# Optimization experiments

Measured on AMD Instinct MI355X. Metric: run time of the kernel, lower is better.

Reference implementation:

```python
import jax, jax.numpy as jnp
import numpy as np

B, N, L = 32, 50, 16384  # batch, n_templates, segment length
KT = 4096                # template kernel length


def conv1d(x, w, pad, groups=1):
    # x: [B, Cin, L], w: [Cout, Cin/groups, K] (torch layout)
    return jax.lax.conv_general_dilated(
        x, w, window_strides=(1,), padding=[(pad, pad)],
        dimension_numbers=('NCH', 'OIH', 'NCH'), feature_group_count=groups)


def maxpool3(x):
    # MaxPool1d(kernel=3, stride=3), floor mode (VALID)
    return jax.lax.reduce_window(x, -jnp.inf, jax.lax.max,
                                 (1, 1, 3), (1, 1, 3), 'VALID')


def pad_to(x, m):
    p = (-x.shape[-1]) % m
    pads = ((0, 0),) * (x.ndim - 1) + ((0, p),)
    return jnp.pad(x, pads)


def setup_inputs() -> dict:
    key = jax.random.key(0)
    ks = jax.random.split(key, 12)
    return dict(
        xi=jax.random.normal(ks[0], (B, 2, L), jnp.float32),
        S_t_m12=jax.random.normal(ks[1], (2, 1, L), jnp.float32) * 0.01,
        template=jax.random.normal(ks[2], (N, 2, KT), jnp.float32) * 0.01,
        hh_sqrt=jax.random.uniform(ks[3], (N, 2), jnp.float32) + 0.5,
        W1=jax.random.normal(ks[4], (16, 2, 3), jnp.float32) * 0.1,
        b1=jnp.zeros((16,), jnp.float32),
        W2=jax.random.normal(ks[5], (32, 16, 3), jnp.float32) * 0.1,
        b2=jnp.zeros((32,), jnp.float32),
        W3=jax.random.normal(ks[6], (32, 128), jnp.float32) * 0.1,
        b3=jnp.zeros((32,), jnp.float32),
        W4=jax.random.normal(ks[7], (2, 32), jnp.float32) * 0.1,
        b4=jnp.zeros((2,), jnp.float32),
    )


def reference(xi, S_t_m12, template, hh_sqrt, W1, b1, W2, b2, W3, b3, W4, b4):
    # Whitening matched filter: grouped conv with kernel length L
    y = conv1d(xi, S_t_m12, L - 1, groups=2)          # [B, 2, 2L-1]
    y = pad_to(y, L)                                   # [B, 2, 2L]
    # wrap-fold each channel: reshape(B,2,L).sum over the fold axis
    d_SA = y[:, 0].reshape(-1, 2, L).sum(1)[:, None, :]  # [B,1,L]
    d_SE = y[:, 1].reshape(-1, 2, L).sum(1)[:, None, :]
    h_SA = template[:, 0, :].reshape(-1, 1, KT)          # [N,1,KT]
    h_SE = template[:, 1, :].reshape(-1, 1, KT)
    dh_A = pad_to(conv1d(d_SA, h_SA, KT - 1), L).reshape(-1, N, 2, L).sum(2)  # [B,N,L]
    dh_E = pad_to(conv1d(d_SE, h_SE, KT - 1), L).reshape(-1, N, 2, L).sum(2)
    z = jnp.stack((dh_A, dh_E), -1).transpose(0, 2, 1, 3)  # [B,L,N,2]
    z = z / hh_sqrt                                         # broadcast [N,2]
    z = z.max(axis=1).transpose(0, 2, 1)                    # [B,2,N]
    # small CNN + MLP head
    h = maxpool3(jax.nn.sigmoid(conv1d(z, W1, 0) + b1[None, :, None]))  # [B,16,16]
    h = maxpool3(jax.nn.sigmoid(conv1d(h, W2, 0) + b2[None, :, None]))  # [B,32,4]
    h = h.reshape(h.shape[0], -1)                                        # [B,128]
    h = jax.nn.relu(h @ W3.T + b3)
    return h @ W4.T + b4                                                 # [B,2]
```

## Files before the change

kernel.cpp:

```cpp
#include <hip/hip_runtime.h>
#include <math.h>

#define L_LEN 16384
#define M_LEN 8192
#define KT_LEN 4096
#define BB 32
#define NTPL 50
#define SPEC_STRIDE 8224
#define NSIG 166
#define NT 1024
#define PI_F 3.14159265358979323846f
#define C8 0.92387953251128674f
#define S8 0.38268343236508978f

typedef float cf2 __attribute__((ext_vector_type(2)));


__device__ __forceinline__ cf2 cmul(cf2 a, cf2 b) {
    cf2 byx = __builtin_shufflevector(b, b, 1, 0);
    return (cf2){a.x, a.x} * b + (cf2){-a.y, a.y} * byx;
}
__device__ __forceinline__ cf2 cmulc(cf2 a, cf2 b) {
    return a * (cf2){b.x, b.x} + (cf2){a.y, -a.x} * (cf2){b.y, b.y};
}
template<int SIGN>
__device__ __forceinline__ cf2 rot90(cf2 z) {
    return (SIGN < 0) ? (cf2){z.y, -z.x} : (cf2){-z.y, z.x};
}
template<int SIGN>
__device__ __forceinline__ cf2 ldT(const cf2* __restrict__ T, int idx) {
    cf2 t = T[idx];
    if (SIGN > 0) t.y = -t.y;
    return t;
}

__device__ __forceinline__ int swz(int i) { return i ^ (((i >> 5) & 15) << 1); }

__device__ __forceinline__ int pos8(int f) {
    return ((f & 7) << 10) | (((f >> 3) & 7) << 7) |
           (((f >> 6) & 7) << 4) | (((f >> 9) & 7) << 1) | ((f >> 12) & 1);
}

template<int SIGN>
__device__ __forceinline__ void dft8(cf2 x[8]) {
    const float R2 = 0.70710678118654752f;
    const cf2 w81 = { R2, SIGN * R2 };
    const cf2 w83 = { -R2, SIGN * R2 };
    cf2 u0 = x[0] + x[4], u1 = x[1] + x[5], u2 = x[2] + x[6], u3 = x[3] + x[7];
    cf2 v0 = x[0] - x[4];
    cf2 v1 = cmul(x[1] - x[5], w81);
    cf2 v2 = rot90<SIGN>(x[2] - x[6]);
    cf2 v3 = cmul(x[3] - x[7], w83);
    cf2 t0 = u0 + u2, t2 = u0 - u2;
    cf2 t1 = u1 + u3, t3 = rot90<SIGN>(u1 - u3);
    x[0] = t0 + t1; x[2] = t2 + t3; x[4] = t0 - t1; x[6] = t2 - t3;
    cf2 s0 = v0 + v2, s2 = v0 - v2;
    cf2 s1 = v1 + v3, s3 = rot90<SIGN>(v1 - v3);
    x[1] = s0 + s1; x[3] = s2 + s3; x[5] = s0 - s1; x[7] = s2 - s3;
}

template<int SIGN>
__device__ __forceinline__ void butterfly8(cf2* A, const int idx[8], cf2 w1) {
    cf2 x[8];
    #pragma unroll
    for (int n = 0; n < 8; ++n) x[n] = A[idx[n]];
    dft8<SIGN>(x);
    A[idx[0]] = x[0];
    A[idx[1]] = cmul(x[1], w1);
    const cf2 w2 = cmul(w1, w1);
    A[idx[2]] = cmul(x[2], w2);
    const cf2 w3 = cmul(w1, w2);
    A[idx[3]] = cmul(x[3], w3);
    const cf2 w4 = cmul(w2, w2);
    A[idx[4]] = cmul(x[4], w4);
    A[idx[5]] = cmul(x[5], cmul(w1, w4));
    A[idx[6]] = cmul(x[6], cmul(w2, w4));
    A[idx[7]] = cmul(x[7], cmul(w3, w4));
}


__global__ __launch_bounds__(NT, 8)
void fwd_fft_kernel(const float* __restrict__ xi, const float* __restrict__ w,
                    const float* __restrict__ tmpl, cf2* __restrict__ Tw,
                    cf2* __restrict__ spec) {
    __shared__ __attribute__((aligned(16))) cf2 A[M_LEN];
    const int sig = blockIdx.x;
    const int tid = threadIdx.x;

    if (sig >= NSIG) {
        const int k = (sig - NSIG) * NT + tid;
        const int quad = k >> 12, mm = k & 4095;
        float s, c; __sincosf(PI_F * (float)mm / 8192.f, &s, &c);
        cf2 v;
        if      (quad == 0) v = (cf2){ c, -s};
        else if (quad == 1) v = (cf2){-s, -c};
        else if (quad == 2) v = (cf2){-c,  s};
        else                v = (cf2){ s,  c};
        Tw[k] = v;
        return;
    }

    const float* src;
    int nre;
    if (sig < 64)      { src = xi   + sig * L_LEN;         nre = L_LEN; }
    else if (sig < 66) { src = w    + (sig - 64) * L_LEN;  nre = L_LEN; }
    else               { src = tmpl + (sig - 66) * KT_LEN; nre = KT_LEN; }
    const bool isW = (sig >= 64 && sig < 66);
    const int nc = nre >> 1;
    const float4* s4 = (const float4*)src;
    const int g0 = tid ^ ((tid >> 4) & 15);
    #pragma unroll
    for (int m = 0; m < 4; ++m) {
        const int u = 2*tid + 2048*m;
        float4 vv = (u < nc) ? s4[tid + 1024*m] : make_float4(0.f, 0.f, 0.f, 0.f);
        ((float4*)A)[g0 + 1024*m] = vv;
    }
    __syncthreads();

    {
        int idx[8]; const int b0 = swz(tid);
        #pragma unroll
        for (int n = 0; n < 8; ++n) idx[n] = b0 + 1024*n;
        float sn, cs; __sincosf(-PI_F * (float)(2*tid) / 8192.f, &sn, &cs);
        butterfly8<-1>(A, idx, (cf2){cs, sn});
    }
    __syncthreads();
    {
        const int blk = tid >> 7, j = tid & 127, jb = blk*1024;
        const int jsw = j ^ (((j >> 5) & 3) << 1);
        int idx[8];
        #pragma unroll
        for (int n = 0; n < 8; ++n) idx[n] = jb + 128*n + (jsw ^ ((n & 3) << 3));
        float sn, cs; __sincosf(-PI_F * (float)(16*j) / 8192.f, &sn, &cs);
        butterfly8<-1>(A, idx, (cf2){cs, sn});
    }
    __syncthreads();
    {
        const int blk = tid >> 4, j = tid & 15;
        const int base = blk*128 + j, bx = (blk & 3) << 3;
        int idx[8];
        #pragma unroll
        for (int n = 0; n < 8; ++n) idx[n] = (base + 16*n) ^ bx ^ ((n >> 1) << 1);
        float sn, cs; __sincosf(-PI_F * (float)(128*j) / 8192.f, &sn, &cs);
        butterfly8<-1>(A, idx, (cf2){cs, sn});
    }
    __syncthreads();
    {
        const int blk = tid >> 1, j = tid & 1;
        const int Xa = ((blk >> 1) & 15) << 1;
        const int base = ((blk << 4) | j) ^ (Xa & 16);
        const int xv = Xa & 14;
        int idx[8];
        #pragma unroll
        for (int n = 0; n < 8; ++n) idx[n] = base + ((2*n) ^ xv);
        cf2 w1 = j ? (cf2){C8, -S8} : (cf2){1.f, 0.f};
        butterfly8<-1>(A, idx, w1);
    }
    __syncthreads();
    #pragma unroll
    for (int m = 0; m < 4; ++m) {
        float4 pq = ((float4*)A)[g0 + 1024*m];
        ((float4*)A)[g0 + 1024*m] = make_float4(pq.x + pq.z, pq.y + pq.w,
                                                pq.x - pq.z, pq.y - pq.w);
    }
    __syncthreads();

    cf2* out = spec + (size_t)sig * SPEC_STRIDE;
    #pragma unroll
    for (int m = 0; m < 8; ++m) {
        const int f = tid + 1024*m;
        const int fb = (M_LEN - f) & (M_LEN - 1);
        cf2 Za = A[swz(pos8(f))];
        cf2 Zb = A[swz(pos8(fb))];
        cf2 E = (cf2){0.5f*(Za.x + Zb.x), 0.5f*(Za.y - Zb.y)};
        cf2 D = (cf2){Za.x - Zb.x, Za.y + Zb.y};
        cf2 O = (cf2){0.5f*D.y, -0.5f*D.x};
        float sn, cs;
        __sincosf(-PI_F * (float)f / 8192.f, &sn, &cs);
        cf2 val = E + (cf2){cs*O.x - sn*O.y, cs*O.y + sn*O.x};
        if (isW) {
            const int k = (4094 * f) & (L_LEN - 1);
            float psn, pcs; __sincosf(-PI_F * (float)k / 8192.f, &psn, &pcs);
            val = cmul((cf2){val.x, -val.y}, (cf2){pcs, psn});
        }
        out[f] = val;
    }
    if (tid == 0) {
        cf2 Za = A[swz(0)];
        cf2 val = (cf2){Za.x - Za.y, 0.f};
        if (isW) {
            val = (cf2){-val.x, 0.f};
        }
        out[M_LEN] = val;
    }
}

__global__ __launch_bounds__(NT, 8)
void inv_fft_kernel(const cf2* __restrict__ spec, const cf2* __restrict__ T,
                    const float* __restrict__ hh, float* __restrict__ zarr) {
    __shared__ __attribute__((aligned(16))) cf2 A[M_LEN];
    const int idx0 = blockIdx.x;
    const int c = idx0 & 1;
    const int n = (idx0 >> 1) % NTPL;
    const int b = idx0 / (2 * NTPL);
    const int tid = threadIdx.x;

    const cf2* Xs = spec + (size_t)(b*2 + c)      * SPEC_STRIDE;
    const cf2* Vs = spec + (size_t)(64 + c)       * SPEC_STRIDE;
    const cf2* Hs = spec + (size_t)(66 + n*2 + c) * SPEC_STRIDE;
    const float4* X4 = (const float4*)Xs;
    const float4* V4 = (const float4*)Vs;
    const float4* H4 = (const float4*)Hs;
    const float4* T4 = (const float4*)T;
    const int g0 = tid ^ ((tid >> 4) & 15);

    #pragma unroll
    for (int m = 0; m < 2; ++m) {
        const int u = 2*tid + 2048*m;
        float4 xf = X4[tid + 1024*m], vf = V4[tid + 1024*m], hf = H4[tid + 1024*m];
        cf2 Sa0 = cmulc(cmul((cf2){xf.x, xf.y}, (cf2){vf.x, vf.y}), (cf2){hf.x, hf.y});
        cf2 Sa1 = cmulc(cmul((cf2){xf.z, xf.w}, (cf2){vf.z, vf.w}), (cf2){hf.z, hf.w});
        cf2 Sb0 = cmulc(cmul(Xs[M_LEN - u],     Vs[M_LEN - u]),     Hs[M_LEN - u]);
        cf2 Sb1 = cmulc(cmul(Xs[M_LEN - 1 - u], Vs[M_LEN - 1 - u]), Hs[M_LEN - 1 - u]);
        float4 tw = T4[tid + 1024*m];
        float cs0 = tw.x, sn0 = -tw.y;
        float Ex0 = 0.5f*(Sa0.x + Sb0.x), Ey0 = 0.5f*(Sa0.y - Sb0.y);
        float Dx0 = Sa0.x - Sb0.x,        Dy0 = Sa0.y + Sb0.y;
        float Ox0 = 0.5f*(cs0*Dx0 - sn0*Dy0), Oy0 = 0.5f*(cs0*Dy0 + sn0*Dx0);
        float cs1 = tw.z, sn1 = -tw.w;
        float Ex1 = 0.5f*(Sa1.x + Sb1.x), Ey1 = 0.5f*(Sa1.y - Sb1.y);
        float Dx1 = Sa1.x - Sb1.x,        Dy1 = Sa1.y + Sb1.y;
        float Ox1 = 0.5f*(cs1*Dx1 - sn1*Dy1), Oy1 = 0.5f*(cs1*Dy1 + sn1*Dx1);
        ((float4*)A)[g0 + 1024*m] = make_float4(Ex0 - Oy0, Ey0 + Ox0,
                                                Ex1 - Oy1, Ey1 + Ox1);
        if (u > 0) A[swz(M_LEN - u)] = (cf2){Ex0 + Oy0, Ox0 - Ey0};
        A[swz(M_LEN - 1 - u)] = (cf2){Ex1 + Oy1, Ox1 - Ey1};
    }
    if (tid == 0) {
        cf2 S = cmulc(cmul(Xs[4096], Vs[4096]), Hs[4096]);
        A[swz(4096)] = (cf2){S.x, -S.y};
    }
    __syncthreads();

    {
        int idx[8]; const int b0 = swz(tid);
        #pragma unroll
        for (int nn = 0; nn < 8; ++nn) idx[nn] = b0 + 1024*nn;
        butterfly8<+1>(A, idx, ldT<+1>(T, 2*tid));
    }
    __syncthreads();
    {
        const int blk = tid >> 7, j = tid & 127, jb = blk*1024;
        const int jsw = j ^ (((j >> 5) & 3) << 1);
        int idx[8];
        #pragma unroll
        for (int nn = 0; nn < 8; ++nn) idx[nn] = jb + 128*nn + (jsw ^ ((nn & 3) << 3));
        butterfly8<+1>(A, idx, ldT<+1>(T, 16*j));
    }
    __syncthreads();
    {
        const int blk = tid >> 4, j = tid & 15;
        const int base = blk*128 + j, bx = (blk & 3) << 3;
        int idx[8];
        #pragma unroll
        for (int nn = 0; nn < 8; ++nn) idx[nn] = (base + 16*nn) ^ bx ^ ((nn >> 1) << 1);
        butterfly8<+1>(A, idx, ldT<+1>(T, 128*j));
    }
    __syncthreads();
    {
        const int blk = tid >> 1, j = tid & 1;
        const int Xa = ((blk >> 1) & 15) << 1;
        const int base = ((blk << 4) | j) ^ (Xa & 16);
        const int xv = Xa & 14;
        int idx[8];
        #pragma unroll
        for (int nn = 0; nn < 8; ++nn) idx[nn] = base + ((2*nn) ^ xv);
        cf2 w1 = j ? (cf2){C8, S8} : (cf2){1.f, 0.f};
        butterfly8<+1>(A, idx, w1);
    }
    __syncthreads();

    float mx = -INFINITY;
    #pragma unroll
    for (int m = 0; m < 4; ++m) {
        float4 pq = ((const float4*)A)[g0 + 1024*m];
        mx = fmaxf(mx, fmaxf(fmaxf(pq.x + pq.z, pq.y + pq.w),
                             fmaxf(pq.x - pq.z, pq.y - pq.w)));
    }
    __syncthreads();
    for (int off = 32; off > 0; off >>= 1)
        mx = fmaxf(mx, __shfl_xor(mx, off));
    const int lane = tid & 63, wv = tid >> 6;
    float* redf = (float*)A;
    if (lane == 0) redf[wv] = mx;
    __syncthreads();
    if (tid == 0) {
        float mm = redf[0];
        for (int i = 1; i < NT/64; ++i) mm = fmaxf(mm, redf[i]);
        zarr[(b*2 + c)*NTPL + n] = mm / ((float)M_LEN * hh[n*2 + c]);
    }
}

__global__ __launch_bounds__(256)
void head_kernel(const float* __restrict__ zarr,
                 const float* __restrict__ W1, const float* __restrict__ b1,
                 const float* __restrict__ W2, const float* __restrict__ b2,
                 const float* __restrict__ W3, const float* __restrict__ b3,
                 const float* __restrict__ W4, const float* __restrict__ b4,
                 float* __restrict__ out) {
    __shared__ float zl[2][NTPL];
    __shared__ float s1[16][48];
    __shared__ float p1[16][16];
    __shared__ float s2[32][14];
    __shared__ float hflat[128];
    __shared__ float h1[32];
    const int b = blockIdx.x, tid = threadIdx.x;

    for (int i = tid; i < 2*NTPL; i += 256) zl[i/NTPL][i%NTPL] = zarr[b*2*NTPL + i];
    __syncthreads();
    for (int i = tid; i < 16*48; i += 256) {
        const int o = i / 48, t = i % 48;
        float acc = b1[o];
        #pragma unroll
        for (int cc = 0; cc < 2; ++cc)
            #pragma unroll
            for (int k = 0; k < 3; ++k)
                acc += zl[cc][t+k] * W1[o*6 + cc*3 + k];
        s1[o][t] = 1.f / (1.f + __expf(-acc));
    }
    __syncthreads();
    for (int i = tid; i < 16*16; i += 256) {
        const int o = i / 16, u = i % 16;
        p1[o][u] = fmaxf(fmaxf(s1[o][3*u], s1[o][3*u+1]), s1[o][3*u+2]);
    }
    __syncthreads();
    for (int i = tid; i < 32*14; i += 256) {
        const int o = i / 14, t = i % 14;
        float acc = b2[o];
        for (int cc = 0; cc < 16; ++cc)
            #pragma unroll
            for (int k = 0; k < 3; ++k)
                acc += p1[cc][t+k] * W2[o*48 + cc*3 + k];
        s2[o][t] = 1.f / (1.f + __expf(-acc));
    }
    __syncthreads();
    for (int i = tid; i < 128; i += 256) {
        const int o = i / 4, u = i % 4;
        hflat[i] = fmaxf(fmaxf(s2[o][3*u], s2[o][3*u+1]), s2[o][3*u+2]);
    }
    __syncthreads();
    if (tid < 32) {
        float acc = b3[tid];
        for (int j = 0; j < 128; ++j) acc += hflat[j] * W3[tid*128 + j];
        h1[tid] = fmaxf(acc, 0.f);
    }
    __syncthreads();
    if (tid < 2) {
        float acc = b4[tid];
        for (int j = 0; j < 32; ++j) acc += h1[j] * W4[tid*32 + j];
        out[b*2 + tid] = acc;
    }
}

extern "C" void kernel_launch(void* const* d_in, const int* in_sizes, int n_in,
                              void* d_out, int out_size, void* d_ws, size_t ws_size,
                              hipStream_t stream) {
    const float* xi   = (const float*)d_in[0];
    const float* Sw   = (const float*)d_in[1];
    const float* tmpl = (const float*)d_in[2];
    const float* hh   = (const float*)d_in[3];
    const float* W1   = (const float*)d_in[4];
    const float* b1   = (const float*)d_in[5];
    const float* W2   = (const float*)d_in[6];
    const float* b2   = (const float*)d_in[7];
    const float* W3   = (const float*)d_in[8];
    const float* b3   = (const float*)d_in[9];
    const float* W4   = (const float*)d_in[10];
    const float* b4   = (const float*)d_in[11];
    float* out = (float*)d_out;

    cf2* T16  = (cf2*)d_ws;
    cf2* spec = T16 + 16384;
    float* zarr = (float*)(spec + (size_t)NSIG * SPEC_STRIDE);

    fwd_fft_kernel<<<dim3(NSIG + 16), dim3(NT), 0, stream>>>(xi, Sw, tmpl, T16, spec);
    inv_fft_kernel<<<dim3(BB * NTPL * 2), dim3(NT), 0, stream>>>(spec, T16, hh, zarr);
    head_kernel<<<dim3(BB), dim3(256), 0, stream>>>(zarr, W1, b1, W2, b2, W3, b3, W4, b4, out);
}
```

Before: 162.3 us.

## Switch inverse FFT to radix-16 with 512 threads and packed complex multiply

```diff
diff --git a/kernel.cpp b/kernel.cpp
--- a/kernel.cpp
+++ b/kernel.cpp
@@ -8,8 +8,11 @@
 #define NTPL 50
 #define SPEC_STRIDE 8224
 #define NSIG 166
-#define NT 1024
+#define NTF 1024
+#define NTI 512
 #define PI_F 3.14159265358979323846f
+#define C16 0.98078528040323044f
+#define S16 0.19509032201612827f
 #define C8 0.92387953251128674f
 #define S8 0.38268343236508978f
 
@@ -17,8 +20,12 @@
 
 
 __device__ __forceinline__ cf2 cmul(cf2 a, cf2 b) {
-    cf2 byx = __builtin_shufflevector(b, b, 1, 0);
-    return (cf2){a.x, a.x} * b + (cf2){-a.y, a.y} * byx;
+    cf2 t, d;
+    asm("v_pk_mul_f32 %0, %1, %2 op_sel:[0,0] op_sel_hi:[0,1]"
+        : "=v"(t) : "v"(a), "v"(b));
+    asm("v_pk_fma_f32 %0, %1, %2, %3 op_sel:[1,1,0] op_sel_hi:[1,0,1] neg_lo:[0,1,0]"
+        : "=v"(d) : "v"(a), "v"(b), "v"(t));
+    return d;
 }
 __device__ __forceinline__ cf2 cmulc(cf2 a, cf2 b) {
     return a * (cf2){b.x, b.x} + (cf2){a.y, -a.x} * (cf2){b.y, b.y};
@@ -39,6 +46,66 @@
 __device__ __forceinline__ int pos8(int f) {
     return ((f & 7) << 10) | (((f >> 3) & 7) << 7) |
            (((f >> 6) & 7) << 4) | (((f >> 9) & 7) << 1) | ((f >> 12) & 1);
+}
+
+template<int SIGN>
+__device__ __forceinline__ void dft16(cf2 x[16]) {
+    const float S = (SIGN < 0) ? -1.f : 1.f;
+    const cf2 w1 = {0.9238795325112867f, S * 0.3826834323650898f};
+    const cf2 w2 = {0.7071067811865476f, S * 0.7071067811865476f};
+    const cf2 w3 = {0.3826834323650898f, S * 0.9238795325112867f};
+    cf2 v[16];
+    #pragma unroll
+    for (int n1 = 0; n1 < 4; ++n1) {
+        cf2 a0 = x[n1], a1 = x[n1+4], a2 = x[n1+8], a3 = x[n1+12];
+        cf2 t0 = a0 + a2, t2 = a0 - a2;
+        cf2 t1 = a1 + a3, t3 = rot90<SIGN>(a1 - a3);
+        cf2 u0 = t0 + t1, u1 = t2 + t3;
+        cf2 u2 = t0 - t1, u3 = t2 - t3;
+        if (n1 == 1) { u1 = cmul(u1, w1); u2 = cmul(u2, w2); u3 = cmul(u3, w3); }
+        else if (n1 == 2) { u1 = cmul(u1, w2); u2 = rot90<SIGN>(u2);
+                            u3 = rot90<SIGN>(cmul(u3, w2)); }
+        else if (n1 == 3) { u1 = cmul(u1, w3); u2 = rot90<SIGN>(cmul(u2, w2));
+                            u3 = -cmul(u3, w1); }
+        v[0*4+n1] = u0; v[1*4+n1] = u1; v[2*4+n1] = u2; v[3*4+n1] = u3;
+    }
+    #pragma unroll
+    for (int r = 0; r < 4; ++r) {
+        cf2 a0 = v[r*4+0], a1 = v[r*4+1], a2 = v[r*4+2], a3 = v[r*4+3];
+        cf2 t0 = a0 + a2, t2 = a0 - a2;
+        cf2 t1 = a1 + a3, t3 = rot90<SIGN>(a1 - a3);
+        x[r]    = t0 + t1; x[r+4]  = t2 + t3;
+        x[r+8]  = t0 - t1; x[r+12] = t2 - t3;
+    }
+}
+
+template<int SIGN>
+__device__ __forceinline__ void butterfly16(cf2* A, const int idx[16], cf2 w1) {
+    cf2 x[16];
+    #pragma unroll
+    for (int n = 0; n < 16; ++n) x[n] = A[idx[n]];
+    dft16<SIGN>(x);
+    A[idx[0]] = x[0];
+    A[idx[1]] = cmul(x[1], w1);
+    const cf2 w2 = cmul(w1, w1);
+    A[idx[2]] = cmul(x[2], w2);
+    const cf2 w3 = cmul(w1, w2);
+    A[idx[3]] = cmul(x[3], w3);
+    const cf2 w4 = cmul(w2, w2);
+    A[idx[4]] = cmul(x[4], w4);
+    A[idx[5]] = cmul(x[5], cmul(w1, w4));
+    A[idx[6]] = cmul(x[6], cmul(w2, w4));
+    A[idx[7]] = cmul(x[7], cmul(w3, w4));
+    const cf2 w8 = cmul(w4, w4);
+    A[idx[8]]  = cmul(x[8],  w8);
+    A[idx[9]]  = cmul(x[9],  cmul(w1, w8));
+    A[idx[10]] = cmul(x[10], cmul(w2, w8));
+    A[idx[11]] = cmul(x[11], cmul(w3, w8));
+    const cf2 w12 = cmul(w4, w8);
+    A[idx[12]] = cmul(x[12], w12);
+    A[idx[13]] = cmul(x[13], cmul(w1, w12));
+    A[idx[14]] = cmul(x[14], cmul(w2, w12));
+    A[idx[15]] = cmul(x[15], cmul(w3, w12));
 }
 
 template<int SIGN>
@@ -78,8 +145,7 @@
     A[idx[7]] = cmul(x[7], cmul(w3, w4));
 }
 
-
-__global__ __launch_bounds__(NT, 8)
+__global__ __launch_bounds__(NTF, 8)
 void fwd_fft_kernel(const float* __restrict__ xi, const float* __restrict__ w,
                     const float* __restrict__ tmpl, cf2* __restrict__ Tw,
                     cf2* __restrict__ spec) {
@@ -88,7 +154,7 @@
     const int tid = threadIdx.x;
 
     if (sig >= NSIG) {
-        const int k = (sig - NSIG) * NT + tid;
+        const int k = (sig - NSIG) * NTF + tid;
         const int quad = k >> 12, mm = k & 4095;
         float s, c; __sincosf(PI_F * (float)mm / 8192.f, &s, &c);
         cf2 v;
@@ -195,7 +261,7 @@
     }
 }
 
-__global__ __launch_bounds__(NT, 8)
+__global__ __launch_bounds__(NTI, 4)
 void inv_fft_kernel(const cf2* __restrict__ spec, const cf2* __restrict__ T,
                     const float* __restrict__ hh, float* __restrict__ zarr) {
     __shared__ __attribute__((aligned(16))) cf2 A[M_LEN];
@@ -215,14 +281,14 @@
     const int g0 = tid ^ ((tid >> 4) & 15);
 
     #pragma unroll
-    for (int m = 0; m < 2; ++m) {
-        const int u = 2*tid + 2048*m;
-        float4 xf = X4[tid + 1024*m], vf = V4[tid + 1024*m], hf = H4[tid + 1024*m];
+    for (int m = 0; m < 4; ++m) {
+        const int u = 2*tid + 1024*m;
+        float4 xf = X4[tid + 512*m], vf = V4[tid + 512*m], hf = H4[tid + 512*m];
         cf2 Sa0 = cmulc(cmul((cf2){xf.x, xf.y}, (cf2){vf.x, vf.y}), (cf2){hf.x, hf.y});
         cf2 Sa1 = cmulc(cmul((cf2){xf.z, xf.w}, (cf2){vf.z, vf.w}), (cf2){hf.z, hf.w});
         cf2 Sb0 = cmulc(cmul(Xs[M_LEN - u],     Vs[M_LEN - u]),     Hs[M_LEN - u]);
         cf2 Sb1 = cmulc(cmul(Xs[M_LEN - 1 - u], Vs[M_LEN - 1 - u]), Hs[M_LEN - 1 - u]);
-        float4 tw = T4[tid + 1024*m];
+        float4 tw = T4[tid + 512*m];
         float cs0 = tw.x, sn0 = -tw.y;
         float Ex0 = 0.5f*(Sa0.x + Sb0.x), Ey0 = 0.5f*(Sa0.y - Sb0.y);
         float Dx0 = Sa0.x - Sb0.x,        Dy0 = Sa0.y + Sb0.y;
@@ -231,8 +297,8 @@
         float Ex1 = 0.5f*(Sa1.x + Sb1.x), Ey1 = 0.5f*(Sa1.y - Sb1.y);
         float Dx1 = Sa1.x - Sb1.x,        Dy1 = Sa1.y + Sb1.y;
         float Ox1 = 0.5f*(cs1*Dx1 - sn1*Dy1), Oy1 = 0.5f*(cs1*Dy1 + sn1*Dx1);
-        ((float4*)A)[g0 + 1024*m] = make_float4(Ex0 - Oy0, Ey0 + Ox0,
-                                                Ex1 - Oy1, Ey1 + Ox1);
+        ((float4*)A)[g0 + 512*m] = make_float4(Ex0 - Oy0, Ey0 + Ox0,
+                                               Ex1 - Oy1, Ey1 + Ox1);
         if (u > 0) A[swz(M_LEN - u)] = (cf2){Ex0 + Oy0, Ox0 - Ey0};
         A[swz(M_LEN - 1 - u)] = (cf2){Ex1 + Oy1, Ox1 - Ey1};
     }
@@ -243,47 +309,35 @@
     __syncthreads();
 
     {
-        int idx[8]; const int b0 = swz(tid);
-        #pragma unroll
-        for (int nn = 0; nn < 8; ++nn) idx[nn] = b0 + 1024*nn;
-        butterfly8<+1>(A, idx, ldT<+1>(T, 2*tid));
-    }
-    __syncthreads();
-    {
-        const int blk = tid >> 7, j = tid & 127, jb = blk*1024;
-        const int jsw = j ^ (((j >> 5) & 3) << 1);
-        int idx[8];
-        #pragma unroll
-        for (int nn = 0; nn < 8; ++nn) idx[nn] = jb + 128*nn + (jsw ^ ((nn & 3) << 3));
-        butterfly8<+1>(A, idx, ldT<+1>(T, 16*j));
-    }
-    __syncthreads();
-    {
-        const int blk = tid >> 4, j = tid & 15;
-        const int base = blk*128 + j, bx = (blk & 3) << 3;
-        int idx[8];
-        #pragma unroll
-        for (int nn = 0; nn < 8; ++nn) idx[nn] = (base + 16*nn) ^ bx ^ ((nn >> 1) << 1);
-        butterfly8<+1>(A, idx, ldT<+1>(T, 128*j));
+        int idx[16]; const int b0 = swz(tid);
+        #pragma unroll
+        for (int nn = 0; nn < 16; ++nn) idx[nn] = b0 + 512*nn;
+        butterfly16<+1>(A, idx, ldT<+1>(T, 2*tid));
+    }
+    __syncthreads();
+    {
+        const int blk = tid >> 5, j = tid & 31, jb = blk*512;
+        int idx[16];
+        #pragma unroll
+        for (int nn = 0; nn < 16; ++nn) idx[nn] = jb + 32*nn + (j ^ (2*nn));
+        butterfly16<+1>(A, idx, ldT<+1>(T, 32*j));
     }
     __syncthreads();
     {
         const int blk = tid >> 1, j = tid & 1;
-        const int Xa = ((blk >> 1) & 15) << 1;
-        const int base = ((blk << 4) | j) ^ (Xa & 16);
-        const int xv = Xa & 14;
-        int idx[8];
-        #pragma unroll
-        for (int nn = 0; nn < 8; ++nn) idx[nn] = base + ((2*nn) ^ xv);
-        cf2 w1 = j ? (cf2){C8, S8} : (cf2){1.f, 0.f};
-        butterfly8<+1>(A, idx, w1);
+        const int xv = (blk & 15) << 1, b3 = blk*32 + j;
+        int idx[16];
+        #pragma unroll
+        for (int nn = 0; nn < 16; ++nn) idx[nn] = b3 + ((2*nn) ^ xv);
+        cf2 w1 = j ? (cf2){C16, S16} : (cf2){1.f, 0.f};
+        butterfly16<+1>(A, idx, w1);
     }
     __syncthreads();
 
     float mx = -INFINITY;
     #pragma unroll
-    for (int m = 0; m < 4; ++m) {
-        float4 pq = ((const float4*)A)[g0 + 1024*m];
+    for (int m = 0; m < 8; ++m) {
+        float4 pq = ((const float4*)A)[g0 + 512*m];
         mx = fmaxf(mx, fmaxf(fmaxf(pq.x + pq.z, pq.y + pq.w),
                              fmaxf(pq.x - pq.z, pq.y - pq.w)));
     }
@@ -296,7 +350,7 @@
     __syncthreads();
     if (tid == 0) {
         float mm = redf[0];
-        for (int i = 1; i < NT/64; ++i) mm = fmaxf(mm, redf[i]);
+        for (int i = 1; i < NTI/64; ++i) mm = fmaxf(mm, redf[i]);
         zarr[(b*2 + c)*NTPL + n] = mm / ((float)M_LEN * hh[n*2 + c]);
     }
 }
@@ -383,7 +437,7 @@
     cf2* spec = T16 + 16384;
     float* zarr = (float*)(spec + (size_t)NSIG * SPEC_STRIDE);
 
-    fwd_fft_kernel<<<dim3(NSIG + 16), dim3(NT), 0, stream>>>(xi, Sw, tmpl, T16, spec);
-    inv_fft_kernel<<<dim3(BB * NTPL * 2), dim3(NT), 0, stream>>>(spec, T16, hh, zarr);
+    fwd_fft_kernel<<<dim3(NSIG + 16), dim3(NTF), 0, stream>>>(xi, Sw, tmpl, T16, spec);
+    inv_fft_kernel<<<dim3(BB * NTPL * 2), dim3(NTI), 0, stream>>>(spec, T16, hh, zarr);
     head_kernel<<<dim3(BB), dim3(256), 0, stream>>>(zarr, W1, b1, W2, b2, W3, b3, W4, b4, out);
 }
```

Result: faster. 155.5 us (-4.2%).
